# Optimization experiments

Measured on AMD Instinct MI355X. Metric: run time of the kernel, lower is better.

Reference implementation:

```python
import jax, jax.numpy as jnp
import numpy as np

D_MODEL = 1024
NHEAD = 16
DIM_HEAD = D_MODEL // NHEAD  # 64
SCALE = DIM_HEAD ** -0.5


def _rope_freqs():
    # freqs list = 10000^(-i/32) for i in 0..31 (len == dim_head//2), then cat [f, -f]
    half = 10000.0 ** (-jnp.arange(DIM_HEAD // 2, dtype=jnp.float32) / (DIM_HEAD // 2))
    return jnp.concatenate([half, -half], axis=0)  # [dim_head]


def _rotate_half(t):
    t1, t2 = jnp.split(t, 2, axis=-1)
    return jnp.concatenate([t2, t1], axis=-1)


def setup_inputs() -> dict:
    key = jax.random.key(0)
    ks = jax.random.split(key, 6)
    B, S = 4, 2048
    x = jax.random.normal(ks[0], (B, S, D_MODEL), dtype=jnp.float32)
    p = jnp.broadcast_to(jnp.arange(S, dtype=jnp.int32), (B, S))
    lim_qkv = (1.0 / D_MODEL) ** 0.5
    Wqkv_w = jax.random.uniform(ks[1], (3 * D_MODEL, D_MODEL), jnp.float32, -lim_qkv, lim_qkv)
    Wqkv_b = jax.random.uniform(ks[2], (3 * D_MODEL,), jnp.float32, -lim_qkv, lim_qkv)
    Wo_w = jax.random.uniform(ks[3], (D_MODEL, D_MODEL), jnp.float32, -lim_qkv, lim_qkv)
    Wo_b = jax.random.uniform(ks[4], (D_MODEL,), jnp.float32, -lim_qkv, lim_qkv)
    return {"x": x, "p": p, "Wqkv_w": Wqkv_w, "Wqkv_b": Wqkv_b, "Wo_w": Wo_w, "Wo_b": Wo_b}


def reference(x, p, Wqkv_w, Wqkv_b, Wo_w, Wo_b):
    B, S, D = x.shape
    qkv = (x @ Wqkv_w.T + Wqkv_b).reshape(B, S, 3, NHEAD, DIM_HEAD)
    # torch: transpose(3,1) -> (B, H, 3, S, Dh), unbind dim=2
    q = jnp.transpose(qkv[:, :, 0], (0, 2, 1, 3))  # [B,H,S,Dh]
    k = jnp.transpose(qkv[:, :, 1], (0, 2, 1, 3))
    v = jnp.transpose(qkv[:, :, 2], (0, 2, 1, 3))
    freqs = _rope_freqs()
    ang = p[..., None].astype(jnp.float32) * freqs  # [B,S,Dh]
    cos = jnp.cos(ang)[:, None]  # [B,1,S,Dh] broadcasts over heads
    sin = jnp.sin(ang)[:, None]
    q = q * cos + _rotate_half(q) * sin
    k = k * cos + _rotate_half(k) * sin
    scores = jnp.einsum("bhqd,bhkd->bhqk", q, k) * SCALE
    attn = jax.nn.softmax(scores, axis=-1)
    out = jnp.einsum("bhqk,bhkd->bhqd", attn, v)
    out = jnp.transpose(out, (0, 2, 1, 3)).reshape(B, S, D)
    return out @ Wo_w.T + Wo_b
```

## Files before the change

kernel.cpp:

```cpp
#include <hip/hip_runtime.h>
#include <hip/hip_bf16.h>
#include <cmath>

constexpr int D_MODEL = 1024;
constexpr int NHEAD   = 16;
constexpr int DH      = 64;
constexpr int BATCH   = 4;
constexpr int SEQ     = 2048;
constexpr int TOKENS  = BATCH * SEQ;
constexpr float SCALE = 0.125f;
constexpr float QSF   = 0.125f * 1.44269504088896340736f;

typedef __attribute__((ext_vector_type(8))) short bf16x8;
typedef __attribute__((ext_vector_type(4))) short short4v;
typedef __attribute__((ext_vector_type(4))) float f32x4;

__device__ inline short f2bf(float f) {
    union { float f; unsigned u; } v; v.f = f;
    unsigned r = v.u + 0x7FFFu + ((v.u >> 16) & 1u);
    return (short)(r >> 16);
}
__device__ inline float bf2f(short s) {
    union { float f; unsigned u; } v;
    v.u = ((unsigned)(unsigned short)s) << 16;
    return v.f;
}
__device__ inline void llds16(const void* g, void* l) {
    __builtin_amdgcn_global_load_lds(
        (const __attribute__((address_space(1))) unsigned*)g,
        (__attribute__((address_space(3))) unsigned*)l, 16, 0, 0);
}

constexpr int N8_X    = TOKENS * 1024 / 8;
constexpr int N8_WQKV = 3072 * 1024 / 8;
constexpr int N8_WO   = 1024 * 1024 / 8;

__global__ __launch_bounds__(256) void cvt3_bf16_kernel(
    const float* __restrict__ sx, const float* __restrict__ sq,
    const float* __restrict__ so,
    short* __restrict__ dx, short* __restrict__ dq, short* __restrict__ dо_)
{
    int i = blockIdx.x * blockDim.x + threadIdx.x;
    const float* src; short* dst; int off;
    if (i < N8_X)                  { src = sx; dst = dx;  off = i; }
    else if (i < N8_X + N8_WQKV)   { src = sq; dst = dq;  off = i - N8_X; }
    else                           { src = so; dst = dо_; off = i - N8_X - N8_WQKV; }
    const float4* s = (const float4*)src + (size_t)off * 2;
    float4 a = s[0], b = s[1];
    bf16x8 v;
    v[0] = f2bf(a.x); v[1] = f2bf(a.y); v[2] = f2bf(a.z); v[3] = f2bf(a.w);
    v[4] = f2bf(b.x); v[5] = f2bf(b.y); v[6] = f2bf(b.z); v[7] = f2bf(b.w);
    *(bf16x8*)(dst + (size_t)off * 8) = v;
}

template<int OUT_BF16>
__global__ __launch_bounds__(256) void gemm_mfma_kernel(
    const short* __restrict__ A, const short* __restrict__ B,
    const float* __restrict__ bias, void* __restrict__ C,
    int M, int N, int K)
{
    __shared__ short As[128 * 64];
    __shared__ short Bs[128 * 64];
    const int tid  = threadIdx.x;
    const int w    = tid >> 6;
    const int lane = tid & 63;
    const int q16  = lane & 15;
    const int quad = lane >> 4;
    const int wm   = (w & 1) * 64;
    const int wn   = (w >> 1) * 64;
    const int bm   = blockIdx.x * 128;
    const int bn   = blockIdx.y * 128;

    const int srow = w * 32 + (lane >> 3);
    const int kcs  = lane & 7;

    f32x4 acc[4][4];
    #pragma unroll
    for (int i = 0; i < 4; i++)
        #pragma unroll
        for (int j = 0; j < 4; j++) acc[i][j] = (f32x4){0.f, 0.f, 0.f, 0.f};

    for (int k0 = 0; k0 < K; k0 += 64) {
        __syncthreads();
        #pragma unroll
        for (int i = 0; i < 4; i++) {
            int row = srow + i * 8;
            int kc  = kcs ^ (row & 7);
            const short* ga = A + (size_t)(bm + row) * K + k0 + kc * 8;
            const short* gb = B + (size_t)(bn + row) * K + k0 + kc * 8;
            short* la = &As[(w * 32 + i * 8) * 64];
            short* lb = &Bs[(w * 32 + i * 8) * 64];
            llds16(ga, la);
            llds16(gb, lb);
        }
        __syncthreads();
        #pragma unroll
        for (int ks = 0; ks < 2; ks++) {
            bf16x8 af[4], bfr[4];
            #pragma unroll
            for (int t = 0; t < 4; t++) {
                int ra = wm + t * 16 + q16;
                int ca = (ks * 4 + quad) ^ (ra & 7);
                af[t]  = *(const bf16x8*)&As[ra * 64 + ca * 8];
                int rb = wn + t * 16 + q16;
                int cb = (ks * 4 + quad) ^ (rb & 7);
                bfr[t] = *(const bf16x8*)&Bs[rb * 64 + cb * 8];
            }
            #pragma unroll
            for (int mb = 0; mb < 4; mb++)
                #pragma unroll
                for (int nb = 0; nb < 4; nb++)
                    acc[mb][nb] = __builtin_amdgcn_mfma_f32_16x16x32_bf16(
                        af[mb], bfr[nb], acc[mb][nb], 0, 0, 0);
        }
    }

    #pragma unroll
    for (int nb = 0; nb < 4; nb++) {
        const int cn = bn + wn + nb * 16 + q16;
        const float bv = bias[cn];
        #pragma unroll
        for (int mb = 0; mb < 4; mb++) {
            const int rm = bm + wm + mb * 16 + quad * 4;
            #pragma unroll
            for (int r = 0; r < 4; r++) {
                float v = acc[mb][nb][r] + bv;
                if (OUT_BF16)
                    ((short*)C)[(size_t)(rm + r) * N + cn] = f2bf(v);
                else
                    ((float*)C)[(size_t)(rm + r) * N + cn] = v;
            }
        }
    }
}

__global__ __launch_bounds__(256) void rope_bf16_kernel(
    short* __restrict__ qkv, const int* __restrict__ p)
{
    int idx = blockIdx.x * blockDim.x + threadIdx.x;
    int i   = idx & 31;
    int h   = (idx >> 5) & 15;
    int tok = idx >> 9;
    if (tok >= TOKENS) return;
    float frev = __builtin_amdgcn_exp2f((float)i * -0.4152410118609203f)
                 * 0.15915494309189535f;
    float t = (float)p[tok] * frev;
    t -= floorf(t);
    float sn = __builtin_amdgcn_sinf(t);
    float c  = __builtin_amdgcn_cosf(t);
    short* base = qkv + (size_t)tok * 3072 + h * 64 + i;
    float q1 = bf2f(base[0]),    q2 = bf2f(base[32]);
    base[0]    = f2bf(fmaf(q1, c,  q2 * sn) * QSF);
    base[32]   = f2bf(fmaf(q2, c, -q1 * sn) * QSF);
    float k1 = bf2f(base[1024]), k2 = bf2f(base[1056]);
    base[1024] = f2bf(fmaf(k1, c,  k2 * sn));
    base[1056] = f2bf(fmaf(k2, c, -k1 * sn));
}

__global__ __launch_bounds__(256, 2) void attn_mfma_kernel(
    const short* __restrict__ qkv, short* __restrict__ out)
{
    __shared__ short Ks[2][64 * 64];
    __shared__ short Vs[2][64 * 64];
    __shared__ short Ps[4][16][72];

    const int tid  = threadIdx.x;
    const int w    = tid >> 6;
    const int lane = tid & 63;
    const int q16  = lane & 15;
    const int quad = lane >> 4;
    const int gid  = blockIdx.x;
    const int bh   = gid & 63;
    const int qblk = gid >> 6;
    const int b    = bh >> 4;
    const int h    = bh & 15;
    const int qtok0 = qblk * 256 + w * 64;

    bf16x8 qf[4][2];
    #pragma unroll
    for (int qb = 0; qb < 4; qb++) {
        const short* Qrow =
            qkv + (size_t)(b * SEQ + qtok0 + qb * 16 + q16) * 3072 + h * 64;
        qf[qb][0] = *(const bf16x8*)(Qrow + quad * 8);
        qf[qb][1] = *(const bf16x8*)(Qrow + 32 + quad * 8);
    }

    f32x4 o[4][4];
    #pragma unroll
    for (int qb = 0; qb < 4; qb++)
        #pragma unroll
        for (int md = 0; md < 4; md++) o[qb][md] = (f32x4){0.f, 0.f, 0.f, 0.f};
    float lsum[4] = {0.f, 0.f, 0.f, 0.f};

    const short* Kg = qkv + (size_t)b * SEQ * 3072 + 1024 + h * 64;
    const short* Vg = Kg + 1024;

    const int krow = w * 16 + (lane >> 3);
    const int kc   = (lane & 7) ^ (krow & 7);
    const int vkey = (tid & 31) * 2;
    const int vdb  = (tid >> 5) * 8;

    auto vwrite = [&](int buf, const uint4& a, const uint4& bb) {
        #pragma unroll
        for (int j = 0; j < 8; j++) {
            unsigned lo = (j & 1) ? 0x07060302u : 0x05040100u;
            unsigned sa = (&a.x)[j >> 1], sb = (&bb.x)[j >> 1];
            *(unsigned*)&Vs[buf][(vdb + j) * 64 + (((vkey >> 3) ^ j) << 3) + (vkey & 7)] =
                __builtin_amdgcn_perm(sb, sa, lo);
        }
    };

    {
        llds16(Kg + (size_t)krow * 3072 + kc * 8, &Ks[0][(w * 16) * 64]);
        llds16(Kg + (size_t)(krow + 8) * 3072 + kc * 8, &Ks[0][(w * 16 + 8) * 64]);
        const short* vsrc = Vg + (size_t)vkey * 3072 + vdb;
        uint4 a  = *(const uint4*)vsrc;
        uint4 bb = *(const uint4*)(vsrc + 3072);
        vwrite(0, a, bb);
    }
    __syncthreads();

    int cur = 0;
    for (int t = 0; t < SEQ / 64; t++) {
        uint4 pva, pvb;
        const bool pf = (t < SEQ / 64 - 1);
        if (pf) {
            const int ktn = (t + 1) * 64;
            llds16(Kg + (size_t)(ktn + krow) * 3072 + kc * 8,
                   &Ks[cur ^ 1][(w * 16) * 64]);
            llds16(Kg + (size_t)(ktn + krow + 8) * 3072 + kc * 8,
                   &Ks[cur ^ 1][(w * 16 + 8) * 64]);
            const short* vsrc = Vg + (size_t)(ktn + vkey) * 3072 + vdb;
            pva = *(const uint4*)vsrc;
            pvb = *(const uint4*)(vsrc + 3072);
        }

        bf16x8 af[4][2], av[4][2];
        #pragma unroll
        for (int mb = 0; mb < 4; mb++) {
            #pragma unroll
            for (int ks = 0; ks < 2; ks++) {
                int c = (((ks * 4 + quad) ^ (q16 & 7))) * 8;
                af[mb][ks] = *(const bf16x8*)&Ks[cur][(mb * 16 + q16) * 64 + c];
                av[mb][ks] = *(const bf16x8*)&Vs[cur][(mb * 16 + q16) * 64 + c];
            }
        }

        #pragma unroll
        for (int qb = 0; qb < 4; qb++) {
            f32x4 sc[4];
            #pragma unroll
            for (int mb = 0; mb < 4; mb++) {
                f32x4 c = {0.f, 0.f, 0.f, 0.f};
                c = __builtin_amdgcn_mfma_f32_16x16x32_bf16(af[mb][0], qf[qb][0], c, 0, 0, 0);
                c = __builtin_amdgcn_mfma_f32_16x16x32_bf16(af[mb][1], qf[qb][1], c, 0, 0, 0);
                sc[mb] = c;
            }
            float ltile = 0.f;
            #pragma unroll
            for (int mb = 0; mb < 2; mb++) {
                float p0 = __builtin_amdgcn_exp2f(sc[mb][0]);
                float p1 = __builtin_amdgcn_exp2f(sc[mb][1]);
                float p2 = __builtin_amdgcn_exp2f(sc[mb][2]);
                float p3 = __builtin_amdgcn_exp2f(sc[mb][3]);
                ltile += (p0 + p1) + (p2 + p3);
                unsigned u0 = __float_as_uint(p0) + 0x8000u;
                unsigned u1 = __float_as_uint(p1) + 0x8000u;
                unsigned u2 = __float_as_uint(p2) + 0x8000u;
                unsigned u3 = __float_as_uint(p3) + 0x8000u;
                uint2 pk;
                pk.x = __builtin_amdgcn_perm(u1, u0, 0x07060302);
                pk.y = __builtin_amdgcn_perm(u3, u2, 0x07060302);
                *(uint2*)&Ps[w][q16][mb * 16 + quad * 4] = pk;
            }
            bf16x8 pb0 = *(const bf16x8*)&Ps[w][q16][quad * 8];
            #pragma unroll
            for (int mb = 2; mb < 4; mb++) {
                float p0 = __builtin_amdgcn_exp2f(sc[mb][0]);
                float p1 = __builtin_amdgcn_exp2f(sc[mb][1]);
                float p2 = __builtin_amdgcn_exp2f(sc[mb][2]);
                float p3 = __builtin_amdgcn_exp2f(sc[mb][3]);
                ltile += (p0 + p1) + (p2 + p3);
                unsigned u0 = __float_as_uint(p0) + 0x8000u;
                unsigned u1 = __float_as_uint(p1) + 0x8000u;
                unsigned u2 = __float_as_uint(p2) + 0x8000u;
                unsigned u3 = __float_as_uint(p3) + 0x8000u;
                uint2 pk;
                pk.x = __builtin_amdgcn_perm(u1, u0, 0x07060302);
                pk.y = __builtin_amdgcn_perm(u3, u2, 0x07060302);
                *(uint2*)&Ps[w][q16][mb * 16 + quad * 4] = pk;
            }
            #pragma unroll
            for (int md = 0; md < 4; md++)
                o[qb][md] = __builtin_amdgcn_mfma_f32_16x16x32_bf16(
                    av[md][0], pb0, o[qb][md], 0, 0, 0);
            bf16x8 pb1 = *(const bf16x8*)&Ps[w][q16][32 + quad * 8];
            #pragma unroll
            for (int md = 0; md < 4; md++)
                o[qb][md] = __builtin_amdgcn_mfma_f32_16x16x32_bf16(
                    av[md][1], pb1, o[qb][md], 0, 0, 0);
            lsum[qb] += ltile;
        }

        if (pf) vwrite(cur ^ 1, pva, pvb);
        __syncthreads();
        cur ^= 1;
    }

    #pragma unroll
    for (int qb = 0; qb < 4; qb++) {
        float l = lsum[qb];
        l += __shfl_xor(l, 16);
        l += __shfl_xor(l, 32);
        float inv = 1.f / l;
        short* orow = out + (size_t)(b * SEQ + qtok0 + qb * 16 + q16) * 1024
                      + h * 64 + quad * 4;
        #pragma unroll
        for (int md = 0; md < 4; md++) {
            short4v t;
            t[0] = f2bf(o[qb][md][0] * inv);
            t[1] = f2bf(o[qb][md][1] * inv);
            t[2] = f2bf(o[qb][md][2] * inv);
            t[3] = f2bf(o[qb][md][3] * inv);
            *(short4v*)(orow + md * 16) = t;
        }
    }
}

extern "C" void kernel_launch(void* const* d_in, const int* in_sizes, int n_in,
                              void* d_out, int out_size, void* d_ws, size_t ws_size,
                              hipStream_t stream)
{
    (void)in_sizes; (void)n_in; (void)out_size; (void)ws_size;
    const float* x      = (const float*)d_in[0];
    const int*   p      = (const int*)  d_in[1];
    const float* Wqkv_w = (const float*)d_in[2];
    const float* Wqkv_b = (const float*)d_in[3];
    const float* Wo_w   = (const float*)d_in[4];
    const float* Wo_b   = (const float*)d_in[5];
    float* out = (float*)d_out;

    short* xb     = (short*)d_ws;
    short* wqkvb  = xb + (size_t)TOKENS * 1024;
    short* wob    = wqkvb + (size_t)3072 * 1024;
    short* qkvb   = wob + (size_t)1024 * 1024;
    short* attnob = qkvb + (size_t)TOKENS * 3072;

    dim3 blk(256);

    cvt3_bf16_kernel<<<dim3((N8_X + N8_WQKV + N8_WO) / 256), blk, 0, stream>>>(
        x, Wqkv_w, Wo_w, xb, wqkvb, wob);

    gemm_mfma_kernel<1><<<dim3(TOKENS / 128, 3072 / 128), blk, 0, stream>>>(
        xb, wqkvb, Wqkv_b, qkvb, TOKENS, 3072, 1024);

    rope_bf16_kernel<<<dim3(TOKENS * NHEAD * 32 / 256), blk, 0, stream>>>(qkvb, p);

    attn_mfma_kernel<<<dim3(512), blk, 0, stream>>>(qkvb, attnob);

    gemm_mfma_kernel<0><<<dim3(TOKENS / 128, 1024 / 128), blk, 0, stream>>>(
        attnob, wob, Wo_b, out, TOKENS, 1024, 1024);
}
```

Measured before the change: 281.6 us.

## Build attention P operand in registers via cvt_pk_bf16 and permlane16 swap

Replaces the LDS round-trip used to reshape softmax probabilities into the MFMA B-operand with in-register packing (v_cvt_pk_bf16_f32) and cross-lane exchange (v_permlane16_swap_b32). The V tile's LDS layout is permuted to match the new key ordering of the P fragments. This removes per-iteration LDS stores/loads and the Ps shared buffer, lowering LDS traffic and latency, at the cost of relying on gfx950-specific instructions and a correct key-permutation mapping.

```diff
diff --git a/kernel.cpp b/kernel.cpp
--- a/kernel.cpp
+++ b/kernel.cpp
@@ -14,6 +14,7 @@
 typedef __attribute__((ext_vector_type(8))) short bf16x8;
 typedef __attribute__((ext_vector_type(4))) short short4v;
 typedef __attribute__((ext_vector_type(4))) float f32x4;
+typedef __attribute__((ext_vector_type(4))) unsigned u32x4;
 
 __device__ inline short f2bf(float f) {
     union { float f; unsigned u; } v; v.f = f;
@@ -38,13 +39,13 @@
 __global__ __launch_bounds__(256) void cvt3_bf16_kernel(
     const float* __restrict__ sx, const float* __restrict__ sq,
     const float* __restrict__ so,
-    short* __restrict__ dx, short* __restrict__ dq, short* __restrict__ dо_)
+    short* __restrict__ dx, short* __restrict__ dq, short* __restrict__ dw)
 {
     int i = blockIdx.x * blockDim.x + threadIdx.x;
     const float* src; short* dst; int off;
     if (i < N8_X)                  { src = sx; dst = dx;  off = i; }
     else if (i < N8_X + N8_WQKV)   { src = sq; dst = dq;  off = i - N8_X; }
-    else                           { src = so; dst = dо_; off = i - N8_X - N8_WQKV; }
+    else                           { src = so; dst = dw;  off = i - N8_X - N8_WQKV; }
     const float4* s = (const float4*)src + (size_t)off * 2;
     float4 a = s[0], b = s[1];
     bf16x8 v;
@@ -162,7 +163,6 @@
 {
     __shared__ short Ks[2][64 * 64];
     __shared__ short Vs[2][64 * 64];
-    __shared__ short Ps[4][16][72];
 
     const int tid  = threadIdx.x;
     const int w    = tid >> 6;
@@ -199,13 +199,14 @@
     const int kc   = (lane & 7) ^ (krow & 7);
     const int vkey = (tid & 31) * 2;
     const int vdb  = (tid >> 5) * 8;
+    const int vL   = ((vkey >> 5) << 2) | (((vkey >> 3) & 1) << 1) | ((vkey >> 4) & 1);
 
     auto vwrite = [&](int buf, const uint4& a, const uint4& bb) {
         #pragma unroll
         for (int j = 0; j < 8; j++) {
             unsigned lo = (j & 1) ? 0x07060302u : 0x05040100u;
             unsigned sa = (&a.x)[j >> 1], sb = (&bb.x)[j >> 1];
-            *(unsigned*)&Vs[buf][(vdb + j) * 64 + (((vkey >> 3) ^ j) << 3) + (vkey & 7)] =
+            *(unsigned*)&Vs[buf][(vdb + j) * 64 + ((vL ^ j) << 3) + (vkey & 7)] =
                 __builtin_amdgcn_perm(sb, sa, lo);
         }
     };
@@ -257,6 +258,7 @@
                 sc[mb] = c;
             }
             float ltile = 0.f;
+            unsigned da[4], db[4];
             #pragma unroll
             for (int mb = 0; mb < 2; mb++) {
                 float p0 = __builtin_amdgcn_exp2f(sc[mb][0]);
@@ -264,16 +266,13 @@
                 float p2 = __builtin_amdgcn_exp2f(sc[mb][2]);
                 float p3 = __builtin_amdgcn_exp2f(sc[mb][3]);
                 ltile += (p0 + p1) + (p2 + p3);
-                unsigned u0 = __float_as_uint(p0) + 0x8000u;
-                unsigned u1 = __float_as_uint(p1) + 0x8000u;
-                unsigned u2 = __float_as_uint(p2) + 0x8000u;
-                unsigned u3 = __float_as_uint(p3) + 0x8000u;
-                uint2 pk;
-                pk.x = __builtin_amdgcn_perm(u1, u0, 0x07060302);
-                pk.y = __builtin_amdgcn_perm(u3, u2, 0x07060302);
-                *(uint2*)&Ps[w][q16][mb * 16 + quad * 4] = pk;
-            }
-            bf16x8 pb0 = *(const bf16x8*)&Ps[w][q16][quad * 8];
+                asm("v_cvt_pk_bf16_f32 %0, %1, %2" : "=v"(da[mb]) : "v"(p0), "v"(p1));
+                asm("v_cvt_pk_bf16_f32 %0, %1, %2" : "=v"(db[mb]) : "v"(p2), "v"(p3));
+            }
+            asm("v_permlane16_swap_b32 %0, %1" : "+v"(da[0]), "+v"(da[1]));
+            asm("v_permlane16_swap_b32 %0, %1" : "+v"(db[0]), "+v"(db[1]));
+            union { u32x4 u; bf16x8 v; } pb0;
+            pb0.u = (u32x4){da[0], db[0], da[1], db[1]};
             #pragma unroll
             for (int mb = 2; mb < 4; mb++) {
                 float p0 = __builtin_amdgcn_exp2f(sc[mb][0]);
@@ -281,24 +280,21 @@
                 float p2 = __builtin_amdgcn_exp2f(sc[mb][2]);
                 float p3 = __builtin_amdgcn_exp2f(sc[mb][3]);
                 ltile += (p0 + p1) + (p2 + p3);
-                unsigned u0 = __float_as_uint(p0) + 0x8000u;
-                unsigned u1 = __float_as_uint(p1) + 0x8000u;
-                unsigned u2 = __float_as_uint(p2) + 0x8000u;
-                unsigned u3 = __float_as_uint(p3) + 0x8000u;
-                uint2 pk;
-                pk.x = __builtin_amdgcn_perm(u1, u0, 0x07060302);
-                pk.y = __builtin_amdgcn_perm(u3, u2, 0x07060302);
-                *(uint2*)&Ps[w][q16][mb * 16 + quad * 4] = pk;
+                asm("v_cvt_pk_bf16_f32 %0, %1, %2" : "=v"(da[mb]) : "v"(p0), "v"(p1));
+                asm("v_cvt_pk_bf16_f32 %0, %1, %2" : "=v"(db[mb]) : "v"(p2), "v"(p3));
             }
             #pragma unroll
             for (int md = 0; md < 4; md++)
                 o[qb][md] = __builtin_amdgcn_mfma_f32_16x16x32_bf16(
-                    av[md][0], pb0, o[qb][md], 0, 0, 0);
-            bf16x8 pb1 = *(const bf16x8*)&Ps[w][q16][32 + quad * 8];
+                    av[md][0], pb0.v, o[qb][md], 0, 0, 0);
+            asm("v_permlane16_swap_b32 %0, %1" : "+v"(da[2]), "+v"(da[3]));
+            asm("v_permlane16_swap_b32 %0, %1" : "+v"(db[2]), "+v"(db[3]));
+            union { u32x4 u; bf16x8 v; } pb1;
+            pb1.u = (u32x4){da[2], db[2], da[3], db[3]};
             #pragma unroll
             for (int md = 0; md < 4; md++)
                 o[qb][md] = __builtin_amdgcn_mfma_f32_16x16x32_bf16(
-                    av[md][1], pb1, o[qb][md], 0, 0, 0);
+                    av[md][1], pb1.v, o[qb][md], 0, 0, 0);
             lsum[qb] += ltile;
         }
 
```

After: 272.6 us. 1.03x faster.
